# Optimization experiments

Hardware: AMD Instinct MI355X
Metric: run time of the kernel (lower is better)

Reference implementation:

```python
import math
import jax, jax.numpy as jnp
import numpy as np

L = 5  # local_context_length
H = 8  # heads


def _local_pool(x, L):
    """Causal local-window softmax pooling.
    For each position i, window = positions [i-L+1, i] (zero-padded at front),
    weights = softmax(x_i . x_window / sqrt(D)), pooled_i = sum_j w_ij * x_window_j.
    x: [B, S, D] -> [B, S, D]."""
    B, S, D = x.shape
    xp = jnp.pad(x, ((0, 0), (L - 1, 0), (0, 0)))          # [B, S+L-1, D]
    idx = jnp.arange(S)[:, None] + jnp.arange(L)[None, :]   # [S, L] window gather indices
    win = xp[:, idx, :]                                     # [B, S, L, D]
    scores = jnp.einsum('bsd,bsld->bsl', x, win) / jnp.asarray(math.sqrt(D), x.dtype)
    w = jax.nn.softmax(scores, axis=-1)                     # [B, S, L]
    return jnp.einsum('bsl,bsld->bsd', w, win)              # [B, S, D]


def setup_inputs() -> dict:
    key0 = jax.random.key(0)
    ks = jax.random.split(key0, 10)
    B, S, D = 4, 2048, 512
    scale = 1.0 / math.sqrt(D)
    return {
        'query': jax.random.normal(ks[0], (B, S, D), jnp.float32),
        'key':   jax.random.normal(ks[1], (B, S, D), jnp.float32),
        'value': jax.random.normal(ks[2], (B, S, D), jnp.float32),
        'mask':  jnp.ones((S, S), jnp.int32),  # dead: forward passes mask=None to attention
        'W_fk':  jax.random.normal(ks[3], (D, D), jnp.float32) * scale,
        'b_fk':  jnp.zeros((D,), jnp.float32),
        'W0':    jax.random.normal(ks[4], (D, D), jnp.float32) * scale,
        'b0':    jnp.zeros((D,), jnp.float32),
        'Wout':  jax.random.normal(ks[5], (D, D), jnp.float32) * scale,
        'bout':  jnp.zeros((D,), jnp.float32),
    }


def reference(query, key, value, mask, W_fk, b_fk, W0, b0, Wout, bout):
    B, S, D = query.shape
    dk = D // H

    q = _local_pool(query, L)                                # [B,S,D]
    k = _local_pool(key @ W_fk + b_fk, L)                    # feature_weight_linear then pool
    v = value @ W0 + b0                                      # linears[0]

    def split(x):  # [B,S,D] -> [B,H,S,dk]
        return x.reshape(B, S, H, dk).transpose(0, 2, 1, 3)

    qh, kh, vh = split(q), split(k), split(v)
    scores = jnp.einsum('bhqd,bhkd->bhqk', qh, kh) / jnp.asarray(math.sqrt(dk), q.dtype)
    p = jax.nn.softmax(scores, axis=-1)                      # mask=None, dropout off (eval)
    x = jnp.einsum('bhqk,bhkd->bhqd', p, vh)
    x = x.transpose(0, 2, 1, 3).reshape(B, S, D)
    return x @ Wout + bout                                   # linears[-1]
```

## Files before the change

### kernel.cpp

```cpp
#include <hip/hip_runtime.h>
#include <hip/hip_bf16.h>
#include <math.h>

#define B_  4
#define S_  2048
#define D_  512
#define H_  8
#define DK_ 64
#define BS_ (B_*S_)

using bf16x8 = __attribute__((ext_vector_type(8))) short;
using f32x4  = __attribute__((ext_vector_type(4))) float;
using f32x16 = __attribute__((ext_vector_type(16))) float;

typedef const __attribute__((address_space(1))) unsigned int gu32;
typedef __attribute__((address_space(3))) unsigned int lu32;

static __device__ inline float bf16f(unsigned short u) {
  union { unsigned u32; float f; } x; x.u32 = (unsigned)u << 16; return x.f;
}
static __device__ inline unsigned pk2(float a, float b) {
  unsigned r;
  asm("v_cvt_pk_bf16_f32 %0, %1, %2" : "=v"(r) : "v"(a), "v"(b));
  return r;
}
static __device__ inline float ex2(float a) {
  return __builtin_amdgcn_exp2f(a);
}

template <int SPLIT, int OUTMODE>
static __device__ __forceinline__ void gemm_body(
    const float* __restrict__ A, const float* __restrict__ W,
    const float* __restrict__ bias, void* __restrict__ Cv,
    int bn, int bm, char* lds) {
  unsigned short (*As)[128][72] = (unsigned short(*)[128][72])lds;
  unsigned short (*Wt)[64][72] =
      (unsigned short(*)[64][72])(lds + (size_t)(SPLIT + 1) * 128 * 72 * 2);
  const int tid = threadIdx.x;
  const int wv = tid >> 6, lane = tid & 63;
  const int c = lane & 15, g = lane >> 4;

  f32x4 acc[2][4];
#pragma unroll
  for (int rt = 0; rt < 2; ++rt)
#pragma unroll
    for (int ds = 0; ds < 4; ++ds) acc[rt][ds] = f32x4{0.f, 0.f, 0.f, 0.f};

  const int arow = tid >> 1, ah = (tid & 1) * 32;
  const int wn = tid & 63, wkg = (tid >> 6) * 16;

  float af[32];
  float wf[16];

  auto LOADT = [&](int k0) {
    const float* ag = A + ((size_t)(bm * 128 + arow)) * D_ + k0 + ah;
#pragma unroll
    for (int i = 0; i < 8; ++i) *(float4*)&af[i * 4] = *(const float4*)(ag + i * 4);
    const float* wg = W + (size_t)(k0 + wkg) * D_ + bn * 64 + wn;
#pragma unroll
    for (int i = 0; i < 16; ++i) wf[i] = wg[(size_t)i * D_];
  };

  auto STORET = [&]() {
#pragma unroll
    for (int grp = 0; grp < 4; ++grp) {
      unsigned h[4], l[4];
#pragma unroll
      for (int p = 0; p < 4; ++p) {
        float f0 = af[grp * 8 + p * 2], f1 = af[grp * 8 + p * 2 + 1];
        h[p] = pk2(f0, f1);
        if constexpr (SPLIT)
          l[p] = pk2(f0 - bf16f((unsigned short)(h[p] & 0xffff)),
                     f1 - bf16f((unsigned short)(h[p] >> 16)));
      }
      uint4 uh; uh.x = h[0]; uh.y = h[1]; uh.z = h[2]; uh.w = h[3];
      *(uint4*)&As[0][arow][ah + grp * 8] = uh;
      if constexpr (SPLIT) {
        uint4 ul; ul.x = l[0]; ul.y = l[1]; ul.z = l[2]; ul.w = l[3];
        *(uint4*)&As[1][arow][ah + grp * 8] = ul;
      }
    }
#pragma unroll
    for (int grp = 0; grp < 2; ++grp) {
      unsigned h[4], l[4];
#pragma unroll
      for (int p = 0; p < 4; ++p) {
        float f0 = wf[grp * 8 + p * 2], f1 = wf[grp * 8 + p * 2 + 1];
        h[p] = pk2(f0, f1);
        if constexpr (SPLIT)
          l[p] = pk2(f0 - bf16f((unsigned short)(h[p] & 0xffff)),
                     f1 - bf16f((unsigned short)(h[p] >> 16)));
      }
      uint4 uh; uh.x = h[0]; uh.y = h[1]; uh.z = h[2]; uh.w = h[3];
      *(uint4*)&Wt[0][wn][wkg + grp * 8] = uh;
      if constexpr (SPLIT) {
        uint4 ul; ul.x = l[0]; ul.y = l[1]; ul.z = l[2]; ul.w = l[3];
        *(uint4*)&Wt[1][wn][wkg + grp * 8] = ul;
      }
    }
  };

  LOADT(0);
  for (int k0 = 0; k0 < D_; k0 += 64) {
    __syncthreads();
    STORET();
    __syncthreads();
    if (k0 + 64 < D_) LOADT(k0 + 64);

#pragma unroll
    for (int ksub = 0; ksub < 2; ++ksub) {
      bf16x8 bh[2], bl[2];
#pragma unroll
      for (int rt = 0; rt < 2; ++rt) {
        bh[rt] = *(const bf16x8*)&As[0][wv * 32 + rt * 16 + c][ksub * 32 + g * 8];
        if constexpr (SPLIT)
          bl[rt] = *(const bf16x8*)&As[1][wv * 32 + rt * 16 + c][ksub * 32 + g * 8];
      }
#pragma unroll
      for (int ds = 0; ds < 4; ++ds) {
        bf16x8 ah_ = *(const bf16x8*)&Wt[0][ds * 16 + c][ksub * 32 + g * 8];
#pragma unroll
        for (int rt = 0; rt < 2; ++rt)
          acc[rt][ds] = __builtin_amdgcn_mfma_f32_16x16x32_bf16(ah_, bh[rt], acc[rt][ds], 0, 0, 0);
        if constexpr (SPLIT) {
          bf16x8 al_ = *(const bf16x8*)&Wt[1][ds * 16 + c][ksub * 32 + g * 8];
#pragma unroll
          for (int rt = 0; rt < 2; ++rt) {
            acc[rt][ds] = __builtin_amdgcn_mfma_f32_16x16x32_bf16(ah_, bl[rt], acc[rt][ds], 0, 0, 0);
            acc[rt][ds] = __builtin_amdgcn_mfma_f32_16x16x32_bf16(al_, bh[rt], acc[rt][ds], 0, 0, 0);
          }
        }
      }
    }
  }

#pragma unroll
  for (int rt = 0; rt < 2; ++rt) {
    const size_t m = (size_t)bm * 128 + wv * 32 + rt * 16 + c;
#pragma unroll
    for (int ds = 0; ds < 4; ++ds) {
      const int n = bn * 64 + ds * 16 + 4 * g;
      float4 bv = *(const float4*)&bias[n];
      float o0 = acc[rt][ds][0] + bv.x, o1 = acc[rt][ds][1] + bv.y;
      float o2 = acc[rt][ds][2] + bv.z, o3 = acc[rt][ds][3] + bv.w;
      if constexpr (OUTMODE == 1) {
        uint2 p; p.x = pk2(o0, o1); p.y = pk2(o2, o3);
        *(uint2*)((unsigned short*)Cv + m * D_ + n) = p;
      } else if constexpr (OUTMODE == 2) {
        const unsigned u01 = pk2(o0, o1), u23 = pk2(o2, o3);
        unsigned short* base =
            (unsigned short*)Cv + ((size_t)(m >> 11) * D_ + n) * (size_t)S_ + (m & 2047);
        base[0]      = (unsigned short)u01;
        base[S_]     = (unsigned short)(u01 >> 16);
        base[2 * S_] = (unsigned short)u23;
        base[3 * S_] = (unsigned short)(u23 >> 16);
      } else {
        float4 o; o.x = o0; o.y = o1; o.z = o2; o.w = o3;
        *(float4*)((float*)Cv + m * D_ + n) = o;
      }
    }
  }
}

template <int BF16IN>
static __device__ __forceinline__ void pool_body(
    const void* __restrict__ xv, unsigned short* __restrict__ out,
    float oscale, int bid) {
  const int gtid = bid * 256 + threadIdx.x;
  const int wave = gtid >> 6;
  const int lane = gtid & 63;
  const int b = wave / S_, s = wave % S_;
  const int d0 = lane * 8;
  float xi[8];
  float win[5][8];
  if constexpr (BF16IN) {
    const unsigned short* xrow =
        (const unsigned short*)xv + ((size_t)b * S_ + s) * D_ + d0;
    uint4 u = *(const uint4*)xrow;
#pragma unroll
    for (int t = 0; t < 4; ++t) {
      unsigned w_ = ((const unsigned*)&u)[t];
      xi[2 * t] = bf16f((unsigned short)(w_ & 0xffff));
      xi[2 * t + 1] = bf16f((unsigned short)(w_ >> 16));
    }
  } else {
    const float* xrow = (const float*)xv + ((size_t)b * S_ + s) * D_ + d0;
    *(float4*)&xi[0] = *(const float4*)xrow;
    *(float4*)&xi[4] = *(const float4*)(xrow + 4);
  }
  float sc[5];
#pragma unroll
  for (int j = 0; j < 5; ++j) {
    int src = s - 4 + j;
    float part = 0.f;
    if (src >= 0) {
      if constexpr (BF16IN) {
        const unsigned short* wr =
            (const unsigned short*)xv + ((size_t)b * S_ + src) * D_ + d0;
        uint4 u = *(const uint4*)wr;
#pragma unroll
        for (int t = 0; t < 4; ++t) {
          unsigned w_ = ((const unsigned*)&u)[t];
          win[j][2 * t] = bf16f((unsigned short)(w_ & 0xffff));
          win[j][2 * t + 1] = bf16f((unsigned short)(w_ >> 16));
        }
      } else {
        const float* wr = (const float*)xv + ((size_t)b * S_ + src) * D_ + d0;
        *(float4*)&win[j][0] = *(const float4*)wr;
        *(float4*)&win[j][4] = *(const float4*)(wr + 4);
      }
#pragma unroll
      for (int t = 0; t < 8; ++t) part += xi[t] * win[j][t];
    } else {
#pragma unroll
      for (int t = 0; t < 8; ++t) win[j][t] = 0.f;
    }
    sc[j] = part;
  }
#pragma unroll
  for (int off = 1; off < 64; off <<= 1) {
#pragma unroll
    for (int j = 0; j < 5; ++j) sc[j] += __shfl_xor(sc[j], off, 64);
  }
  const float scale = 0.04419417382415922f;
  float m = sc[0] * scale;
#pragma unroll
  for (int j = 1; j < 5; ++j) m = fmaxf(m, sc[j] * scale);
  float w[5], lsum = 0.f;
#pragma unroll
  for (int j = 0; j < 5; ++j) { w[j] = expf(sc[j] * scale - m); lsum += w[j]; }
  const float inv = oscale / lsum;
  float o[8] = {};
#pragma unroll
  for (int j = 0; j < 5; ++j)
#pragma unroll
    for (int t = 0; t < 8; ++t) o[t] += w[j] * win[j][t];
  unsigned short* orow = out + ((size_t)b * S_ + s) * D_;
  uint4 pk;
  pk.x = pk2(o[0] * inv, o[1] * inv);
  pk.y = pk2(o[2] * inv, o[3] * inv);
  pk.z = pk2(o[4] * inv, o[5] * inv);
  pk.w = pk2(o[6] * inv, o[7] * inv);
  *(uint4*)&orow[d0] = pk;
}

__global__ __launch_bounds__(256) void phaseA_kernel(
    const float* __restrict__ key, const float* __restrict__ W_fk,
    const float* __restrict__ b_fk, void* __restrict__ kfk_bf16,
    const float* __restrict__ value, const float* __restrict__ W0,
    const float* __restrict__ b0, void* __restrict__ vT,
    const float* __restrict__ query, unsigned short* __restrict__ qout,
    float qscale) {
  __shared__ __align__(16) char Lraw[27648];
  int bid = blockIdx.x;
  if (bid < 512) {
    gemm_body<0, 1>(key, W_fk, b_fk, kfk_bf16, bid & 7, bid >> 3, Lraw);
  } else if (bid < 1024) {
    bid -= 512;
    gemm_body<0, 2>(value, W0, b0, vT, bid & 7, bid >> 3, Lraw);
  } else {
    pool_body<0>(query, qout, qscale, bid - 1024);
  }
}

__global__ __launch_bounds__(256) void pool_k_kernel(
    const unsigned short* __restrict__ kfk_bf16,
    unsigned short* __restrict__ kout) {
  pool_body<1>(kfk_bf16, kout, 1.0f, blockIdx.x);
}

__global__ __launch_bounds__(256) void gemm_out_kernel(
    const float* __restrict__ x, const float* __restrict__ Wout,
    const float* __restrict__ bout, float* __restrict__ out) {
  __shared__ __align__(16) char Lraw[55296];
  gemm_body<1, 0>(x, Wout, bout, out, blockIdx.x & 7, blockIdx.x >> 3, Lraw);
}

__global__ __launch_bounds__(256, 3) void attn_mfma32_kernel(
    const unsigned short* __restrict__ q, const unsigned short* __restrict__ k,
    const unsigned short* __restrict__ vt, float* __restrict__ x) {
  const int bid = (blockIdx.x & 7) * 128 + (blockIdx.x >> 3);
  const int qb = bid & 31;
  const int h  = (bid >> 5) & 7;
  const int b  = bid >> 8;
  const int tid = threadIdx.x;
  const int w = tid >> 6, l = tid & 63;
  const int ql = l & 31, hi = l >> 5;
  const int wq = w & 1, wh = w >> 1;

  __shared__ __align__(16) unsigned short Kb[2][2][4096];
  __shared__ __align__(16) unsigned short Vb[2][4096];

  bf16x8 Qf[4];
  {
    const unsigned short* qg =
        q + ((size_t)b * S_ + qb * 64 + wq * 32 + ql) * D_ + h * 64 + hi * 8;
#pragma unroll
    for (int f = 0; f < 4; ++f) Qf[f] = *(const bf16x8*)(qg + f * 16);
  }

  f32x16 accO[2] = {};
  float m = -INFINITY, lsum = 0.f;

  const int lr8 = l >> 3, lc = l & 7;
  const unsigned short* kg =
      k + ((size_t)b * S_ + wh * 1024 + wq * 32 + lr8) * D_ + h * 64 + ((lc ^ lr8) << 3);
  const unsigned short* vg =
      vt + ((size_t)b * D_ + h * 64 + wq * 32 + lr8) * (size_t)S_ + wh * 1024 + ((lc ^ lr8) << 3);

  auto ISSUE_K = [&](int t, int bf) {
    const unsigned short* kp = kg + (size_t)t * 64 * D_;
    char* dk = (char*)&Kb[bf][wh][0] + wq * 4096;
#pragma unroll
    for (int j = 0; j < 4; ++j)
      __builtin_amdgcn_global_load_lds((gu32*)(kp + (size_t)j * 8 * D_),
                                       (lu32*)(dk + j * 1024), 16, 0, 0);
  };
  auto ISSUE_V = [&](int t) {
    const unsigned short* vp = vg + t * 64;
    char* dv = (char*)&Vb[wh][0] + wq * 4096;
#pragma unroll
    for (int j = 0; j < 4; ++j)
      __builtin_amdgcn_global_load_lds((gu32*)(vp + (size_t)j * 8 * S_),
                                       (lu32*)(dv + j * 1024), 16, 0, 0);
  };

  ISSUE_K(0, 0);
  ISSUE_V(0);
  asm volatile("s_waitcnt vmcnt(0)" ::: "memory");
  __builtin_amdgcn_s_barrier();
  __builtin_amdgcn_sched_barrier(0);

  int cur = 0;
  for (int kt = 0; kt < 16; ++kt) {
    const char* KsB = (const char*)&Kb[cur][wh][0];
    const char* VtB = (const char*)&Vb[wh][0];

    f32x16 sA = {}, sB = {};
    __builtin_amdgcn_s_setprio(1);
#pragma unroll
    for (int f = 0; f < 4; ++f) {
      bf16x8 a0 = *(const bf16x8*)(KsB + ((ql * 128 + f * 32 + hi * 16) ^ ((ql & 7) << 4)));
      bf16x8 a1 = *(const bf16x8*)(KsB + (((ql + 32) * 128 + f * 32 + hi * 16) ^ ((ql & 7) << 4)));
      sA = __builtin_amdgcn_mfma_f32_32x32x16_bf16(a0, Qf[f], sA, 0, 0, 0);
      sB = __builtin_amdgcn_mfma_f32_32x32x16_bf16(a1, Qf[f], sB, 0, 0, 0);
    }
    __builtin_amdgcn_s_setprio(0);

    if (kt + 1 < 16) ISSUE_K(kt + 1, cur ^ 1);
    __builtin_amdgcn_sched_barrier(0);

    float mx[8];
#pragma unroll
    for (int r = 0; r < 8; ++r)
      mx[r] = fmaxf(fmaxf(sA[r], sA[r + 8]), fmaxf(sB[r], sB[r + 8]));
    mx[0] = fmaxf(mx[0], mx[4]); mx[1] = fmaxf(mx[1], mx[5]);
    mx[2] = fmaxf(mx[2], mx[6]); mx[3] = fmaxf(mx[3], mx[7]);
    mx[0] = fmaxf(fmaxf(mx[0], mx[1]), fmaxf(mx[2], mx[3]));
    const float mt = fmaxf(mx[0], __shfl_xor(mx[0], 32, 64));
    if (!__all(mt <= m + 10.0f)) {
      const float mn = fmaxf(m, mt);
      const float corr = ex2(m - mn);
      m = mn;
      lsum *= corr;
#pragma unroll
      for (int dt = 0; dt < 2; ++dt)
#pragma unroll
        for (int r = 0; r < 16; ++r) accO[dt][r] *= corr;
    }

    unsigned WA[8], WB[8];
    float s0 = 0.f, s1 = 0.f, s2 = 0.f, s3 = 0.f;
#pragma unroll
    for (int t = 0; t < 4; ++t) {
      float a0 = ex2(sA[4 * t + 0] - m), a1 = ex2(sA[4 * t + 1] - m);
      float a2 = ex2(sA[4 * t + 2] - m), a3 = ex2(sA[4 * t + 3] - m);
      WA[2 * t] = pk2(a0, a1); WA[2 * t + 1] = pk2(a2, a3);
      s0 += a0 + a1; s1 += a2 + a3;
      float b0 = ex2(sB[4 * t + 0] - m), b1 = ex2(sB[4 * t + 1] - m);
      float b2 = ex2(sB[4 * t + 2] - m), b3 = ex2(sB[4 * t + 3] - m);
      WB[2 * t] = pk2(b0, b1); WB[2 * t + 1] = pk2(b2, b3);
      s2 += b0 + b1; s3 += b2 + b3;
    }
    lsum += (s0 + s1) + (s2 + s3);

    if (kt + 1 < 16) asm volatile("s_waitcnt vmcnt(4)" ::: "memory");
    else             asm volatile("s_waitcnt vmcnt(0)" ::: "memory");
    __builtin_amdgcn_s_barrier();
    __builtin_amdgcn_sched_barrier(0);

#pragma unroll
    for (int kc = 0; kc < 4; ++kc) {
      unsigned w0 = (kc < 2) ? WA[(kc & 1) * 4 + 0] : WB[(kc & 1) * 4 + 0];
      unsigned w1 = (kc < 2) ? WA[(kc & 1) * 4 + 1] : WB[(kc & 1) * 4 + 1];
      unsigned w2 = (kc < 2) ? WA[(kc & 1) * 4 + 2] : WB[(kc & 1) * 4 + 2];
      unsigned w3 = (kc < 2) ? WA[(kc & 1) * 4 + 3] : WB[(kc & 1) * 4 + 3];
      asm volatile("v_permlane32_swap_b32 %0, %1" : "+v"(w0), "+v"(w2));
      asm volatile("v_permlane32_swap_b32 %0, %1" : "+v"(w1), "+v"(w3));
      union { unsigned u[4]; bf16x8 v8; } pb;
      pb.u[0] = w0; pb.u[1] = w1; pb.u[2] = w2; pb.u[3] = w3;
      __builtin_amdgcn_s_setprio(1);
#pragma unroll
      for (int dt = 0; dt < 2; ++dt) {
        const int vrow = dt * 32 + ql;
        bf16x8 va = *(const bf16x8*)(VtB + ((vrow * 128 + kc * 32 + hi * 16) ^ ((ql & 7) << 4)));
        accO[dt] = __builtin_amdgcn_mfma_f32_32x32x16_bf16(va, pb.v8, accO[dt], 0, 0, 0);
      }
      __builtin_amdgcn_s_setprio(0);
    }

    __builtin_amdgcn_s_barrier();
    __builtin_amdgcn_sched_barrier(0);
    if (kt + 1 < 16) {
      ISSUE_V(kt + 1);
      asm volatile("s_waitcnt vmcnt(4)" ::: "memory");
      __builtin_amdgcn_s_barrier();
      __builtin_amdgcn_sched_barrier(0);
    }
    cur ^= 1;
  }

  float lw = lsum + __shfl_xor(lsum, 32, 64);
  __syncthreads();
  float* cb = (float*)Kb + (size_t)wq * 2176 + (size_t)l * 34;
  if (wh == 1) {
#pragma unroll
    for (int dt = 0; dt < 2; ++dt)
#pragma unroll
      for (int r = 0; r < 16; ++r) cb[dt * 16 + r] = accO[dt][r];
    cb[32] = m; cb[33] = lw;
  }
  __syncthreads();
  if (wh == 0) {
    const float m1 = cb[32], l1 = cb[33];
    const float mn = fmaxf(m, m1);
    const float a0 = ex2(m - mn), a1 = ex2(m1 - mn);
    const float inv = 1.f / (lw * a0 + l1 * a1);
    float* xrow = x + ((size_t)b * S_ + qb * 64 + wq * 32 + ql) * D_ + h * 64;
#pragma unroll
    for (int dt = 0; dt < 2; ++dt)
#pragma unroll
      for (int g0 = 0; g0 < 4; ++g0) {
        float4 o;
        o.x = (accO[dt][4 * g0 + 0] * a0 + cb[dt * 16 + 4 * g0 + 0] * a1) * inv;
        o.y = (accO[dt][4 * g0 + 1] * a0 + cb[dt * 16 + 4 * g0 + 1] * a1) * inv;
        o.z = (accO[dt][4 * g0 + 2] * a0 + cb[dt * 16 + 4 * g0 + 2] * a1) * inv;
        o.w = (accO[dt][4 * g0 + 3] * a0 + cb[dt * 16 + 4 * g0 + 3] * a1) * inv;
        *(float4*)&xrow[dt * 32 + hi * 4 + g0 * 8] = o;
      }
  }
}

extern "C" void kernel_launch(void* const* d_in, const int* in_sizes, int n_in,
                              void* d_out, int out_size, void* d_ws, size_t ws_size,
                              hipStream_t stream) {
  const float* query = (const float*)d_in[0];
  const float* key   = (const float*)d_in[1];
  const float* value = (const float*)d_in[2];
  const float* W_fk = (const float*)d_in[4];
  const float* b_fk = (const float*)d_in[5];
  const float* W0   = (const float*)d_in[6];
  const float* b0   = (const float*)d_in[7];
  const float* Wout = (const float*)d_in[8];
  const float* bout = (const float*)d_in[9];
  float* out = (float*)d_out;

  char* ws = (char*)d_ws;
  unsigned short* kfk_bf16 = (unsigned short*)ws;
  float* x_f32   = (float*)(ws + (16u << 20));
  unsigned short* k_bf16  = (unsigned short*)(ws + (32u << 20));
  unsigned short* vT_bf16 = (unsigned short*)(ws + (40u << 20));
  unsigned short* q_bf16  = (unsigned short*)(ws + (48u << 20));

  const float qscale = 0.125f * 1.4426950408889634f;

  phaseA_kernel<<<3072, 256, 0, stream>>>(key, W_fk, b_fk, kfk_bf16,
                                          value, W0, b0, vT_bf16,
                                          query, q_bf16, qscale);
  pool_k_kernel<<<2048, 256, 0, stream>>>(kfk_bf16, k_bf16);
  attn_mfma32_kernel<<<dim3(B_ * H_ * (S_ / 64)), 256, 0, stream>>>(
      q_bf16, k_bf16, vT_bf16, x_f32);
  gemm_out_kernel<<<512, 256, 0, stream>>>(x_f32, Wout, bout, out);
}
```

Measured before the change: 150.3 us.

## Restructure attention into 8-wave blocks sharing K/V tiles across 256 query rows

The attention kernel now uses 512-thread blocks where each of 8 waves owns 32 query rows, so every K/V tile loaded into LDS is shared by 256 queries instead of 64. It drops the split-KV across wave pairs and the LDS-based merge of partial softmax states, and each wave walks all 32 key tiles. K and V for the next tile are prefetched together into double buffers at the top of the iteration, leaving one wait and barrier per step. This cuts global K/V traffic and merge overhead. In exchange the grid shrinks to 256 blocks, which lowers occupancy and parallelism on a GPU with many CUs, and each wave runs twice as many serial iterations.

```diff
diff --git a/kernel.cpp b/kernel.cpp
--- a/kernel.cpp
+++ b/kernel.cpp
@@ -276,25 +276,24 @@
   gemm_body<1, 0>(x, Wout, bout, out, blockIdx.x & 7, blockIdx.x >> 3, Lraw);
 }
 
-__global__ __launch_bounds__(256, 3) void attn_mfma32_kernel(
+__global__ __launch_bounds__(512) void attn8_kernel(
     const unsigned short* __restrict__ q, const unsigned short* __restrict__ k,
     const unsigned short* __restrict__ vt, float* __restrict__ x) {
-  const int bid = (blockIdx.x & 7) * 128 + (blockIdx.x >> 3);
-  const int qb = bid & 31;
-  const int h  = (bid >> 5) & 7;
-  const int b  = bid >> 8;
+  const int bid = (blockIdx.x & 7) * 32 + (blockIdx.x >> 3);
+  const int qb = bid & 7;
+  const int h  = (bid >> 3) & 7;
+  const int b  = bid >> 6;
   const int tid = threadIdx.x;
   const int w = tid >> 6, l = tid & 63;
   const int ql = l & 31, hi = l >> 5;
-  const int wq = w & 1, wh = w >> 1;
-
-  __shared__ __align__(16) unsigned short Kb[2][2][4096];
+
+  __shared__ __align__(16) unsigned short Kb[2][4096];
   __shared__ __align__(16) unsigned short Vb[2][4096];
 
   bf16x8 Qf[4];
   {
     const unsigned short* qg =
-        q + ((size_t)b * S_ + qb * 64 + wq * 32 + ql) * D_ + h * 64 + hi * 8;
+        q + ((size_t)b * S_ + qb * 256 + w * 32 + ql) * D_ + h * 64 + hi * 8;
 #pragma unroll
     for (int f = 0; f < 4; ++f) Qf[f] = *(const bf16x8*)(qg + f * 16);
   }
@@ -302,39 +301,31 @@
   f32x16 accO[2] = {};
   float m = -INFINITY, lsum = 0.f;
 
-  const int lr8 = l >> 3, lc = l & 7;
+  const int r_ = tid >> 3, c_ = tid & 7;
+  const int swz = (c_ ^ (r_ & 7)) << 3;
   const unsigned short* kg =
-      k + ((size_t)b * S_ + wh * 1024 + wq * 32 + lr8) * D_ + h * 64 + ((lc ^ lr8) << 3);
+      k + ((size_t)b * S_ + r_) * D_ + h * 64 + swz;
   const unsigned short* vg =
-      vt + ((size_t)b * D_ + h * 64 + wq * 32 + lr8) * (size_t)S_ + wh * 1024 + ((lc ^ lr8) << 3);
-
-  auto ISSUE_K = [&](int t, int bf) {
-    const unsigned short* kp = kg + (size_t)t * 64 * D_;
-    char* dk = (char*)&Kb[bf][wh][0] + wq * 4096;
-#pragma unroll
-    for (int j = 0; j < 4; ++j)
-      __builtin_amdgcn_global_load_lds((gu32*)(kp + (size_t)j * 8 * D_),
-                                       (lu32*)(dk + j * 1024), 16, 0, 0);
+      vt + ((size_t)b * D_ + h * 64 + r_) * (size_t)S_ + swz;
+
+  auto ISSUE = [&](int t, int bf) {
+    __builtin_amdgcn_global_load_lds((gu32*)(kg + (size_t)t * 64 * D_),
+                                     (lu32*)((char*)&Kb[bf][0] + tid * 16), 16, 0, 0);
+    __builtin_amdgcn_global_load_lds((gu32*)(vg + t * 64),
+                                     (lu32*)((char*)&Vb[bf][0] + tid * 16), 16, 0, 0);
   };
-  auto ISSUE_V = [&](int t) {
-    const unsigned short* vp = vg + t * 64;
-    char* dv = (char*)&Vb[wh][0] + wq * 4096;
-#pragma unroll
-    for (int j = 0; j < 4; ++j)
-      __builtin_amdgcn_global_load_lds((gu32*)(vp + (size_t)j * 8 * S_),
-                                       (lu32*)(dv + j * 1024), 16, 0, 0);
-  };
-
-  ISSUE_K(0, 0);
-  ISSUE_V(0);
+
+  ISSUE(0, 0);
   asm volatile("s_waitcnt vmcnt(0)" ::: "memory");
   __builtin_amdgcn_s_barrier();
   __builtin_amdgcn_sched_barrier(0);
 
   int cur = 0;
-  for (int kt = 0; kt < 16; ++kt) {
-    const char* KsB = (const char*)&Kb[cur][wh][0];
-    const char* VtB = (const char*)&Vb[wh][0];
+  for (int kt = 0; kt < 32; ++kt) {
+    if (kt + 1 < 32) ISSUE(kt + 1, cur ^ 1);
+    __builtin_amdgcn_sched_barrier(0);
+    const char* KsB = (const char*)&Kb[cur][0];
+    const char* VtB = (const char*)&Vb[cur][0];
 
     f32x16 sA = {}, sB = {};
     __builtin_amdgcn_s_setprio(1);
@@ -346,9 +337,6 @@
       sB = __builtin_amdgcn_mfma_f32_32x32x16_bf16(a1, Qf[f], sB, 0, 0, 0);
     }
     __builtin_amdgcn_s_setprio(0);
-
-    if (kt + 1 < 16) ISSUE_K(kt + 1, cur ^ 1);
-    __builtin_amdgcn_sched_barrier(0);
 
     float mx[8];
 #pragma unroll
@@ -384,11 +372,6 @@
     }
     lsum += (s0 + s1) + (s2 + s3);
 
-    if (kt + 1 < 16) asm volatile("s_waitcnt vmcnt(4)" ::: "memory");
-    else             asm volatile("s_waitcnt vmcnt(0)" ::: "memory");
-    __builtin_amdgcn_s_barrier();
-    __builtin_amdgcn_sched_barrier(0);
-
 #pragma unroll
     for (int kc = 0; kc < 4; ++kc) {
       unsigned w0 = (kc < 2) ? WA[(kc & 1) * 4 + 0] : WB[(kc & 1) * 4 + 0];
@@ -409,46 +392,26 @@
       __builtin_amdgcn_s_setprio(0);
     }
 
+    asm volatile("s_waitcnt vmcnt(0)" ::: "memory");
     __builtin_amdgcn_s_barrier();
     __builtin_amdgcn_sched_barrier(0);
-    if (kt + 1 < 16) {
-      ISSUE_V(kt + 1);
-      asm volatile("s_waitcnt vmcnt(4)" ::: "memory");
-      __builtin_amdgcn_s_barrier();
-      __builtin_amdgcn_sched_barrier(0);
-    }
     cur ^= 1;
   }
 
-  float lw = lsum + __shfl_xor(lsum, 32, 64);
-  __syncthreads();
-  float* cb = (float*)Kb + (size_t)wq * 2176 + (size_t)l * 34;
-  if (wh == 1) {
-#pragma unroll
-    for (int dt = 0; dt < 2; ++dt)
-#pragma unroll
-      for (int r = 0; r < 16; ++r) cb[dt * 16 + r] = accO[dt][r];
-    cb[32] = m; cb[33] = lw;
-  }
-  __syncthreads();
-  if (wh == 0) {
-    const float m1 = cb[32], l1 = cb[33];
-    const float mn = fmaxf(m, m1);
-    const float a0 = ex2(m - mn), a1 = ex2(m1 - mn);
-    const float inv = 1.f / (lw * a0 + l1 * a1);
-    float* xrow = x + ((size_t)b * S_ + qb * 64 + wq * 32 + ql) * D_ + h * 64;
-#pragma unroll
-    for (int dt = 0; dt < 2; ++dt)
-#pragma unroll
-      for (int g0 = 0; g0 < 4; ++g0) {
-        float4 o;
-        o.x = (accO[dt][4 * g0 + 0] * a0 + cb[dt * 16 + 4 * g0 + 0] * a1) * inv;
-        o.y = (accO[dt][4 * g0 + 1] * a0 + cb[dt * 16 + 4 * g0 + 1] * a1) * inv;
-        o.z = (accO[dt][4 * g0 + 2] * a0 + cb[dt * 16 + 4 * g0 + 2] * a1) * inv;
-        o.w = (accO[dt][4 * g0 + 3] * a0 + cb[dt * 16 + 4 * g0 + 3] * a1) * inv;
-        *(float4*)&xrow[dt * 32 + hi * 4 + g0 * 8] = o;
-      }
-  }
+  const float ltot = lsum + __shfl_xor(lsum, 32, 64);
+  const float inv = 1.f / ltot;
+  float* xrow = x + ((size_t)b * S_ + qb * 256 + w * 32 + ql) * D_ + h * 64;
+#pragma unroll
+  for (int dt = 0; dt < 2; ++dt)
+#pragma unroll
+    for (int g0 = 0; g0 < 4; ++g0) {
+      float4 o;
+      o.x = accO[dt][4 * g0 + 0] * inv;
+      o.y = accO[dt][4 * g0 + 1] * inv;
+      o.z = accO[dt][4 * g0 + 2] * inv;
+      o.w = accO[dt][4 * g0 + 3] * inv;
+      *(float4*)&xrow[dt * 32 + hi * 4 + g0 * 8] = o;
+    }
 }
 
 extern "C" void kernel_launch(void* const* d_in, const int* in_sizes, int n_in,
@@ -478,7 +441,7 @@
                                           value, W0, b0, vT_bf16,
                                           query, q_bf16, qscale);
   pool_k_kernel<<<2048, 256, 0, stream>>>(kfk_bf16, k_bf16);
-  attn_mfma32_kernel<<<dim3(B_ * H_ * (S_ / 64)), 256, 0, stream>>>(
+  attn8_kernel<<<dim3(B_ * H_ * (S_ / 256)), 512, 0, stream>>>(
       q_bf16, k_bf16, vT_bf16, x_f32);
   gemm_out_kernel<<<512, 256, 0, stream>>>(x_f32, Wout, bout, out);
 }
```

New measurement: 151.2 us. Within noise of the previous version (+0.6%).
